# Optimization experiments

Hardware: AMD Instinct MI355X
Metric: run time of the kernel (lower is better)

Reference implementation:

```python
import jax, jax.numpy as jnp
import numpy as np

BETA = 0.25

def setup_inputs() -> dict:
    key = jax.random.key(0)
    k1, k2 = jax.random.split(key)
    x = jax.random.normal(k1, (16, 32, 32, 256), dtype=jnp.float32)
    embed = jax.random.normal(k2, (256, 8192), dtype=jnp.float32)
    return {"x": x, "embed": embed}

def reference(x, embed):
    dim = embed.shape[0]
    flatten = x.reshape(-1, dim)  # [N, dim]
    # squared L2 distance to each code: ||f||^2 - 2 f.e + ||e||^2 -> [N, n_embed]
    dist = (jnp.sum(flatten * flatten, axis=1, keepdims=True)
            - 2.0 * (flatten @ embed)
            + jnp.sum(embed * embed, axis=0, keepdims=True))
    ind = jnp.argmin(dist, axis=1)  # == argmax(-dist)
    embed_ind = ind.reshape(x.shape[:-1])  # [B, H, W]
    codebook = embed.T  # [n_embed, dim]
    quantize = codebook[embed_ind]  # gather -> [B, H, W, dim]
    diff = jnp.mean((jax.lax.stop_gradient(quantize) - x) ** 2)
    commit_loss = jnp.mean((quantize - jax.lax.stop_gradient(x)) ** 2)
    diff = diff + commit_loss * BETA
    quantize = x + jax.lax.stop_gradient(quantize - x)  # straight-through
    return quantize, diff, embed_ind
```

## Files before the change

### kernel.cpp

```cpp
#include <hip/hip_runtime.h>

static constexpr int DIM   = 256;
static constexpr int NCODE = 8192;
static constexpr int NROWS = 16384;

typedef __bf16 bf16x8 __attribute__((ext_vector_type(8)));
typedef float  f32x4  __attribute__((ext_vector_type(4)));

__device__ __forceinline__ void top2_insert(float& v0, int& i0, float& v1, int& i1,
                                            float s, int si) {
    if (s < v0) { v1 = v0; i1 = i0; v0 = s; i0 = si; }
    else if (s < v1) { v1 = s; i1 = si; }
}
__device__ __forceinline__ void top2_merge(float& v0, int& i0, float& v1, int& i1,
                                           float b0, int bi0, float b1, int bi1) {
    if (b0 < v0) {
        if (b1 < v0) { v0 = b0; i0 = bi0; v1 = b1; i1 = bi1; }
        else         { v1 = v0; i1 = i0;  v0 = b0; i0 = bi0; }
    } else if (b0 < v1) { v1 = b0; i1 = bi0; }
}

__global__ __launch_bounds__(256) void prep_kernel(
    const float* __restrict__ x, const float* __restrict__ embed,
    ushort* __restrict__ xb, ushort* __restrict__ eb16,
    float* __restrict__ ebT32, float* __restrict__ e2)
{
    __shared__ float tile[64][65];
    const int b = blockIdx.x;
    const int t = threadIdx.x;

    if (b < 2048) {
        int i = b * 256 + t;
        const float4* xp = (const float4*)x + (size_t)i * 2;
        float4 a = xp[0], v = xp[1];
        bf16x8 o;
        o[0] = (__bf16)a.x; o[1] = (__bf16)a.y; o[2] = (__bf16)a.z; o[3] = (__bf16)a.w;
        o[4] = (__bf16)v.x; o[5] = (__bf16)v.y; o[6] = (__bf16)v.z; o[7] = (__bf16)v.w;
        ((bf16x8*)xb)[i] = o;
    } else if (b < 2560) {
        const int eb = b - 2048;
        const int c00 = (eb & 127) * 64;
        const int k0  = (eb >> 7) * 64;
        const int tc  = t & 63, tr4 = t >> 6;
        #pragma unroll
        for (int i = 0; i < 16; ++i) {
            int r = i * 4 + tr4;
            tile[r][tc] = embed[(size_t)(k0 + r) * NCODE + c00 + tc];
        }
        __syncthreads();
        const int cl = t >> 2;
        const int kq = t & 3;
        float vals[16];
        #pragma unroll
        for (int j = 0; j < 16; ++j) vals[j] = tile[kq * 16 + j][cl];
        float* d32 = ebT32 + (size_t)(c00 + cl) * DIM + k0 + kq * 16;
        #pragma unroll
        for (int j = 0; j < 4; ++j)
            *(float4*)(d32 + j * 4) = make_float4(vals[j*4], vals[j*4+1],
                                                  vals[j*4+2], vals[j*4+3]);
        bf16x8 h0, h1;
        #pragma unroll
        for (int j = 0; j < 8; ++j) { h0[j] = (__bf16)vals[j]; h1[j] = (__bf16)vals[8 + j]; }
        ushort* d16 = eb16 + (size_t)(c00 + cl) * DIM + k0 + kq * 16;
        *(bf16x8*)d16 = h0;
        *(bf16x8*)(d16 + 8) = h1;
    } else {
        int j = (b - 2560) * 256 + t;
        float s = 0.f;
        for (int k = 0; k < DIM; ++k) {
            float v = embed[(size_t)k * NCODE + j];
            s = __fadd_rn(s, __fmul_rn(v, v));
        }
        e2[j] = s;
    }
}

__global__ __launch_bounds__(512, 1) void gemm_top2_kernel(
    const ushort* __restrict__ xb,
    const ushort* __restrict__ eb,
    const float* __restrict__ e2g,
    uint2* __restrict__ scratch)
{
    __shared__ ushort Bs[32768];
    __shared__ ushort As[2][16384];
    __shared__ uint4  ldsM[4][64];

    const int t       = threadIdx.x;
    const int chunk   = blockIdx.x >> 2;
    const int rg      = blockIdx.x & 3;
    const int c0      = chunk * 128;
    const int rowbase = rg * 4096;

    const int wid = t >> 6, lane = t & 63;
    const int wr  = wid >> 2, wc = wid & 3;
    const int lr  = lane & 15, g = lane >> 4;

    {
        const char* bb = (const char*)(eb + (size_t)c0 * DIM);
        uint4 breg[8];
        #pragma unroll
        for (int i = 0; i < 8; ++i)
            breg[i] = *(const uint4*)(bb + i * 8192 + t * 16);
        const char* ab = (const char*)(xb + (size_t)rowbase * DIM);
        uint4 areg[4];
        #pragma unroll
        for (int i = 0; i < 4; ++i)
            areg[i] = *(const uint4*)(ab + i * 8192 + t * 16);
        #pragma unroll
        for (int i = 0; i < 8; ++i) {
            int o = i * 8192 + t * 16;
            int code = o >> 9, kg = (o >> 4) & 31;
            *(uint4*)((char*)Bs + kg * 2048 + (((code ^ kg) & 127) << 4)) = breg[i];
        }
        #pragma unroll
        for (int i = 0; i < 4; ++i) {
            int o = i * 8192 + t * 16;
            int row = o >> 9, kg = (o >> 4) & 31;
            *(uint4*)((char*)As[0] + kg * 1024 + (((row ^ kg) & 63) << 4)) = areg[i];
        }
    }
    __syncthreads();

    bf16x8 bq[2][8];
    #pragma unroll
    for (int cf = 0; cf < 2; ++cf) {
        #pragma unroll
        for (int ks = 0; ks < 8; ++ks) {
            int code = wc * 32 + cf * 16 + lr;
            int kg   = ks * 4 + g;
            bq[cf][ks] = *(const bf16x8*)((char*)Bs + kg * 2048 +
                                          (((code ^ kg) & 127) << 4));
        }
    }

    float e2v[2][4];
    #pragma unroll
    for (int cf = 0; cf < 2; ++cf)
        #pragma unroll
        for (int reg = 0; reg < 4; ++reg)
            e2v[cf][reg] = e2g[c0 + wc * 32 + cf * 16 + g * 4 + reg];

    int cur = 0;
    for (int tt = 0; tt < 64; ++tt) {
        uint4 nreg[4];
        if (tt < 63) {
            const char* an = (const char*)(xb + (size_t)(rowbase + (tt + 1) * 64) * DIM);
            #pragma unroll
            for (int i = 0; i < 4; ++i)
                nreg[i] = *(const uint4*)(an + i * 8192 + t * 16);
        }

        f32x4 acc[2][2];
        #pragma unroll
        for (int cf = 0; cf < 2; ++cf)
            #pragma unroll
            for (int rf = 0; rf < 2; ++rf) acc[cf][rf] = (f32x4){0.f, 0.f, 0.f, 0.f};

        const char* Ab = (const char*)As[cur];
        #pragma unroll
        for (int ks = 0; ks < 8; ++ks) {
            bf16x8 af[2];
            #pragma unroll
            for (int rf = 0; rf < 2; ++rf) {
                int row = wr * 32 + rf * 16 + lr;
                int kg  = ks * 4 + g;
                af[rf] = *(const bf16x8*)(Ab + kg * 1024 + (((row ^ kg) & 63) << 4));
            }
            #pragma unroll
            for (int cf = 0; cf < 2; ++cf)
                #pragma unroll
                for (int rf = 0; rf < 2; ++rf)
                    acc[cf][rf] = __builtin_amdgcn_mfma_f32_16x16x32_bf16(
                        bq[cf][ks], af[rf], acc[cf][rf], 0, 0, 0);
        }

        #pragma unroll
        for (int rf = 0; rf < 2; ++rf) {
            float v0 = __builtin_inff(), v1 = __builtin_inff();
            int   i0 = -1, i1 = -1;
            #pragma unroll
            for (int cf = 0; cf < 2; ++cf) {
                #pragma unroll
                for (int reg = 0; reg < 4; ++reg) {
                    float sv = __builtin_fmaf(-2.f, acc[cf][rf][reg], e2v[cf][reg]);
                    top2_insert(v0, i0, v1, i1, sv,
                                c0 + wc * 32 + cf * 16 + g * 4 + reg);
                }
            }
            #pragma unroll
            for (int m = 16; m <= 32; m <<= 1) {
                float b0 = __shfl_xor(v0, m), b1 = __shfl_xor(v1, m);
                int  bi0 = __shfl_xor(i0, m), bi1 = __shfl_xor(i1, m);
                top2_merge(v0, i0, v1, i1, b0, bi0, b1, bi1);
            }
            if (g == 0)
                ldsM[wc][wr * 32 + rf * 16 + lr] =
                    make_uint4(__float_as_uint(v0), (unsigned)i0,
                               __float_as_uint(v1), (unsigned)i1);
        }
        __syncthreads();

        if (t < 64) {
            uint4 E = ldsM[0][t];
            float v0 = __uint_as_float(E.x), v1 = __uint_as_float(E.z);
            int   i0 = (int)E.y,             i1 = (int)E.w;
            #pragma unroll
            for (int k = 1; k < 4; ++k) {
                uint4 F = ldsM[k][t];
                top2_merge(v0, i0, v1, i1, __uint_as_float(F.x), (int)F.y,
                           __uint_as_float(F.z), (int)F.w);
            }
            float delta = v1 - v0;
            unsigned dq = (unsigned)min(63, (int)(delta * 32.f));
            unsigned w2 = (unsigned)i0 | ((unsigned)i1 << 13) | (dq << 26);
            scratch[(size_t)chunk * NROWS + rowbase + tt * 64 + t] =
                make_uint2(__float_as_uint(v0), w2);
        }

        if (tt < 63) {
            #pragma unroll
            for (int i = 0; i < 4; ++i) {
                int o = i * 8192 + t * 16;
                int row = o >> 9, kg = (o >> 4) & 31;
                *(uint4*)((char*)As[cur ^ 1] + kg * 1024 +
                          (((row ^ kg) & 63) << 4)) = nreg[i];
            }
        }
        __syncthreads();
        cur ^= 1;
    }
}

__global__ __launch_bounds__(256) void finalize_kernel(
    const uint2* __restrict__ scratch, const float* __restrict__ x,
    const float* __restrict__ ebT32, const float* __restrict__ e2g,
    float* __restrict__ quant, float* __restrict__ diff, float* __restrict__ ind)
{
    __shared__ float    wmin[4][64];
    __shared__ float    thr[64];
    __shared__ unsigned cnt[64];
    __shared__ unsigned cand[64][12];
    __shared__ unsigned bestIdx[64];
    __shared__ float    partial[4];

    const int t  = threadIdx.x;
    const int w  = t >> 6, l = t & 63;
    const int R0 = blockIdx.x * 64;

    if (t < 64) cnt[t] = 0;

    float m = __builtin_inff();
    #pragma unroll 4
    for (int i = 0; i < 16; ++i) {
        uint2 e = scratch[(size_t)(w * 16 + i) * NROWS + R0 + l];
        m = fminf(m, __uint_as_float(e.x));
    }
    wmin[w][l] = m;
    __syncthreads();
    if (t < 64)
        thr[t] = fminf(fminf(wmin[0][t], wmin[1][t]),
                       fminf(wmin[2][t], wmin[3][t])) + 1.0f;
    __syncthreads();

    const float th = thr[l];
    for (int i = 0; i < 16; ++i) {
        uint2 e = scratch[(size_t)(w * 16 + i) * NROWS + R0 + l];
        float v0 = __uint_as_float(e.x);
        if (v0 <= th) {
            unsigned s = atomicAdd(&cnt[l], 1u);
            if (s < 12) cand[l][s] = e.y & 8191u;
        }
        float v1lo = v0 + (float)((e.y >> 26) & 63u) * 0.03125f;
        if (v1lo <= th) {
            unsigned s = atomicAdd(&cnt[l], 1u);
            if (s < 12) cand[l][s] = (e.y >> 13) & 8191u;
        }
    }
    __syncthreads();

    const int rl = l >> 2, slot = l & 3;
    const int rrow = R0 + w * 16 + rl;
    const int cn = min((int)cnt[w * 16 + rl], 12);
    float best = __builtin_inff();
    unsigned bidx = 0xFFFFFFFFu;
    for (int s = slot; s < cn; s += 4) {
        unsigned idx = cand[w * 16 + rl][s];
        const float* xr = x + (size_t)rrow * DIM;
        const float* er = ebT32 + (size_t)idx * DIM;
        float f2 = 0.f, dot = 0.f;
        for (int k = 0; k < DIM; ++k) {
            float xv = xr[k];
            f2  = __fadd_rn(f2, __fmul_rn(xv, xv));
            dot = __builtin_fmaf(xv, er[k], dot);
        }
        float d = __fadd_rn(__builtin_fmaf(-2.f, dot, f2), e2g[idx]);
        if (d < best || (d == best && idx < bidx)) { best = d; bidx = idx; }
    }
    #pragma unroll
    for (int mm = 1; mm < 4; mm <<= 1) {
        float    od = __shfl_xor(best, mm);
        unsigned oi = (unsigned)__shfl_xor((int)bidx, mm);
        if (od < best || (od == best && oi < bidx)) { best = od; bidx = oi; }
    }
    if (slot == 0) bestIdx[w * 16 + rl] = bidx;
    __syncthreads();

    float accv = 0.f;
    for (int r = 0; r < 64; ++r) {
        const int row2 = R0 + r;
        const unsigned idx = bestIdx[r];
        float xv = x[(size_t)row2 * DIM + t];
        float q  = ebT32[(size_t)idx * DIM + t];
        float dq = __fsub_rn(q, xv);
        quant[(size_t)row2 * DIM + t] = __fadd_rn(xv, dq);
        accv += __fmul_rn(dq, dq);
    }
    #pragma unroll
    for (int off = 32; off >= 1; off >>= 1) accv += __shfl_down(accv, off);
    if (l == 0) partial[w] = accv;
    __syncthreads();
    if (t == 0) {
        float s = (partial[0] + partial[1]) + (partial[2] + partial[3]);
        atomicAdd(diff, s * (1.25f / 4194304.f));
    }
    if (t < 64) ind[R0 + t] = (float)bestIdx[t];
}

extern "C" void kernel_launch(void* const* d_in, const int* in_sizes, int n_in,
                              void* d_out, int out_size, void* d_ws, size_t ws_size,
                              hipStream_t stream)
{
    const float* x     = (const float*)d_in[0];
    const float* embed = (const float*)d_in[1];

    float* out   = (float*)d_out;
    float* quant = out;
    float* diff  = out + 4194304;
    float* ind   = out + 4194305;

    ushort* xb = (ushort*)quant;

    char* w = (char*)d_ws;
    ushort* eb16    = (ushort*)(w);
    float*  ebT32   = (float*) (w + 4194304);
    float*  e2      = (float*) (w + 12582912);
    uint2*  scratch = (uint2*) (w + 12615680);

    prep_kernel<<<2592, 256, 0, stream>>>(x, embed, xb, eb16, ebT32, e2);
    gemm_top2_kernel<<<256, 512, 0, stream>>>(xb, eb16, e2, scratch);
    hipMemsetAsync(diff, 0, sizeof(float), stream);
    finalize_kernel<<<256, 256, 0, stream>>>(scratch, x, ebT32, e2, quant, diff, ind);
}
```

Before: 706.1 us.

## Restructure GEMM to per-wave top2 with direct global A loads

The GEMM kernel is reorganized into 256-thread blocks, two per CU, each holding a 128-code B tile. Each wave keeps 64 codes in registers and reads A fragments straight from global/L2 instead of double-buffered LDS. Each wave now writes its own top-2 result to scratch, which drops the cross-wave LDS merge and its two barriers per tile but doubles the scratch entries the finalize kernel must scan. The fp32 transposed embedding copy is removed, so finalize reads the original embed with strided column accesses, trading prep write traffic for uncoalesced gathers.

```diff
diff --git a/kernel.cpp b/kernel.cpp
--- a/kernel.cpp
+++ b/kernel.cpp
@@ -22,8 +22,7 @@
 
 __global__ __launch_bounds__(256) void prep_kernel(
     const float* __restrict__ x, const float* __restrict__ embed,
-    ushort* __restrict__ xb, ushort* __restrict__ eb16,
-    float* __restrict__ ebT32, float* __restrict__ e2)
+    ushort* __restrict__ xb, ushort* __restrict__ eb16, float* __restrict__ e2)
 {
     __shared__ float tile[64][65];
     const int b = blockIdx.x;
@@ -53,11 +52,6 @@
         float vals[16];
         #pragma unroll
         for (int j = 0; j < 16; ++j) vals[j] = tile[kq * 16 + j][cl];
-        float* d32 = ebT32 + (size_t)(c00 + cl) * DIM + k0 + kq * 16;
-        #pragma unroll
-        for (int j = 0; j < 4; ++j)
-            *(float4*)(d32 + j * 4) = make_float4(vals[j*4], vals[j*4+1],
-                                                  vals[j*4+2], vals[j*4+3]);
         bf16x8 h0, h1;
         #pragma unroll
         for (int j = 0; j < 8; ++j) { h0[j] = (__bf16)vals[j]; h1[j] = (__bf16)vals[8 + j]; }
@@ -75,103 +69,88 @@
     }
 }
 
-__global__ __launch_bounds__(512, 1) void gemm_top2_kernel(
+__global__ __launch_bounds__(256, 2) void gemm_top2_kernel(
     const ushort* __restrict__ xb,
     const ushort* __restrict__ eb,
     const float* __restrict__ e2g,
     uint2* __restrict__ scratch)
 {
     __shared__ ushort Bs[32768];
-    __shared__ ushort As[2][16384];
-    __shared__ uint4  ldsM[4][64];
 
     const int t       = threadIdx.x;
-    const int chunk   = blockIdx.x >> 2;
-    const int rg      = blockIdx.x & 3;
-    const int c0      = chunk * 128;
-    const int rowbase = rg * 4096;
+    const int cpair   = blockIdx.x >> 3;
+    const int rg      = blockIdx.x & 7;
+    const int c0      = cpair * 128;
+    const int rowbase = rg * 2048;
 
     const int wid = t >> 6, lane = t & 63;
-    const int wr  = wid >> 2, wc = wid & 3;
+    const int wr  = wid >> 1, wc = wid & 1;
     const int lr  = lane & 15, g = lane >> 4;
 
     {
         const char* bb = (const char*)(eb + (size_t)c0 * DIM);
-        uint4 breg[8];
-        #pragma unroll
-        for (int i = 0; i < 8; ++i)
-            breg[i] = *(const uint4*)(bb + i * 8192 + t * 16);
-        const char* ab = (const char*)(xb + (size_t)rowbase * DIM);
-        uint4 areg[4];
-        #pragma unroll
-        for (int i = 0; i < 4; ++i)
-            areg[i] = *(const uint4*)(ab + i * 8192 + t * 16);
-        #pragma unroll
-        for (int i = 0; i < 8; ++i) {
-            int o = i * 8192 + t * 16;
+        uint4 breg[16];
+        #pragma unroll
+        for (int i = 0; i < 16; ++i)
+            breg[i] = *(const uint4*)(bb + i * 4096 + t * 16);
+        #pragma unroll
+        for (int i = 0; i < 16; ++i) {
+            int o = i * 4096 + t * 16;
             int code = o >> 9, kg = (o >> 4) & 31;
-            *(uint4*)((char*)Bs + kg * 2048 + (((code ^ kg) & 127) << 4)) = breg[i];
-        }
-        #pragma unroll
-        for (int i = 0; i < 4; ++i) {
-            int o = i * 8192 + t * 16;
-            int row = o >> 9, kg = (o >> 4) & 31;
-            *(uint4*)((char*)As[0] + kg * 1024 + (((row ^ kg) & 63) << 4)) = areg[i];
-        }
-    }
-    __syncthreads();
-
-    bf16x8 bq[2][8];
+            *(uint4*)((char*)Bs + kg * 2048 + (((code + kg) & 127) << 4)) = breg[i];
+        }
+    }
+    __syncthreads();
+
+    bf16x8 bq[4][8];
     #pragma unroll
-    for (int cf = 0; cf < 2; ++cf) {
+    for (int cf = 0; cf < 4; ++cf) {
         #pragma unroll
         for (int ks = 0; ks < 8; ++ks) {
-            int code = wc * 32 + cf * 16 + lr;
-            int kg   = ks * 4 + g;
+            int codeL = wc * 64 + cf * 16 + lr;
+            int kg    = ks * 4 + g;
             bq[cf][ks] = *(const bf16x8*)((char*)Bs + kg * 2048 +
-                                          (((code ^ kg) & 127) << 4));
-        }
-    }
-
-    float e2v[2][4];
+                                          (((codeL + kg) & 127) << 4));
+        }
+    }
+
+    float e2v[4][4];
     #pragma unroll
-    for (int cf = 0; cf < 2; ++cf)
+    for (int cf = 0; cf < 4; ++cf)
         #pragma unroll
         for (int reg = 0; reg < 4; ++reg)
-            e2v[cf][reg] = e2g[c0 + wc * 32 + cf * 16 + g * 4 + reg];
-
-    int cur = 0;
-    for (int tt = 0; tt < 64; ++tt) {
-        uint4 nreg[4];
-        if (tt < 63) {
-            const char* an = (const char*)(xb + (size_t)(rowbase + (tt + 1) * 64) * DIM);
-            #pragma unroll
-            for (int i = 0; i < 4; ++i)
-                nreg[i] = *(const uint4*)(an + i * 8192 + t * 16);
-        }
-
-        f32x4 acc[2][2];
-        #pragma unroll
-        for (int cf = 0; cf < 2; ++cf)
+            e2v[cf][reg] = e2g[c0 + wc * 64 + cf * 16 + g * 4 + reg];
+
+    const char* ab    = (const char*)xb;
+    const int   ccol  = cpair * 2 + wc;
+
+    for (int tt = 0; tt < 32; ++tt) {
+        const int row0 = rowbase + tt * 64 + wr * 32;
+
+        f32x4 acc[4][2];
+        #pragma unroll
+        for (int cf = 0; cf < 4; ++cf)
             #pragma unroll
             for (int rf = 0; rf < 2; ++rf) acc[cf][rf] = (f32x4){0.f, 0.f, 0.f, 0.f};
 
-        const char* Ab = (const char*)As[cur];
-        #pragma unroll
-        for (int ks = 0; ks < 8; ++ks) {
-            bf16x8 af[2];
-            #pragma unroll
-            for (int rf = 0; rf < 2; ++rf) {
-                int row = wr * 32 + rf * 16 + lr;
-                int kg  = ks * 4 + g;
-                af[rf] = *(const bf16x8*)(Ab + kg * 1024 + (((row ^ kg) & 63) << 4));
-            }
-            #pragma unroll
-            for (int cf = 0; cf < 2; ++cf)
+        #pragma unroll
+        for (int half = 0; half < 2; ++half) {
+            bf16x8 af[4][2];
+            #pragma unroll
+            for (int k4 = 0; k4 < 4; ++k4)
                 #pragma unroll
                 for (int rf = 0; rf < 2; ++rf)
-                    acc[cf][rf] = __builtin_amdgcn_mfma_f32_16x16x32_bf16(
-                        bq[cf][ks], af[rf], acc[cf][rf], 0, 0, 0);
+                    af[k4][rf] = *(const bf16x8*)(ab +
+                        (size_t)(row0 + rf * 16 + lr) * 512 +
+                        (half * 4 + k4) * 64 + g * 16);
+            #pragma unroll
+            for (int k4 = 0; k4 < 4; ++k4)
+                #pragma unroll
+                for (int cf = 0; cf < 4; ++cf)
+                    #pragma unroll
+                    for (int rf = 0; rf < 2; ++rf)
+                        acc[cf][rf] = __builtin_amdgcn_mfma_f32_16x16x32_bf16(
+                            bq[cf][half * 4 + k4], af[k4][rf], acc[cf][rf], 0, 0, 0);
         }
 
         #pragma unroll
@@ -179,12 +158,12 @@
             float v0 = __builtin_inff(), v1 = __builtin_inff();
             int   i0 = -1, i1 = -1;
             #pragma unroll
-            for (int cf = 0; cf < 2; ++cf) {
+            for (int cf = 0; cf < 4; ++cf) {
                 #pragma unroll
                 for (int reg = 0; reg < 4; ++reg) {
                     float sv = __builtin_fmaf(-2.f, acc[cf][rf][reg], e2v[cf][reg]);
                     top2_insert(v0, i0, v1, i1, sv,
-                                c0 + wc * 32 + cf * 16 + g * 4 + reg);
+                                c0 + wc * 64 + cf * 16 + g * 4 + reg);
                 }
             }
             #pragma unroll
@@ -193,47 +172,20 @@
                 int  bi0 = __shfl_xor(i0, m), bi1 = __shfl_xor(i1, m);
                 top2_merge(v0, i0, v1, i1, b0, bi0, b1, bi1);
             }
-            if (g == 0)
-                ldsM[wc][wr * 32 + rf * 16 + lr] =
-                    make_uint4(__float_as_uint(v0), (unsigned)i0,
-                               __float_as_uint(v1), (unsigned)i1);
-        }
-        __syncthreads();
-
-        if (t < 64) {
-            uint4 E = ldsM[0][t];
-            float v0 = __uint_as_float(E.x), v1 = __uint_as_float(E.z);
-            int   i0 = (int)E.y,             i1 = (int)E.w;
-            #pragma unroll
-            for (int k = 1; k < 4; ++k) {
-                uint4 F = ldsM[k][t];
-                top2_merge(v0, i0, v1, i1, __uint_as_float(F.x), (int)F.y,
-                           __uint_as_float(F.z), (int)F.w);
+            if (g == 0) {
+                float delta = v1 - v0;
+                unsigned dq = (unsigned)min(63, (int)(delta * 32.f));
+                unsigned w2 = (unsigned)i0 | ((unsigned)i1 << 13) | (dq << 26);
+                scratch[(size_t)ccol * NROWS + row0 + rf * 16 + lr] =
+                    make_uint2(__float_as_uint(v0), w2);
             }
-            float delta = v1 - v0;
-            unsigned dq = (unsigned)min(63, (int)(delta * 32.f));
-            unsigned w2 = (unsigned)i0 | ((unsigned)i1 << 13) | (dq << 26);
-            scratch[(size_t)chunk * NROWS + rowbase + tt * 64 + t] =
-                make_uint2(__float_as_uint(v0), w2);
-        }
-
-        if (tt < 63) {
-            #pragma unroll
-            for (int i = 0; i < 4; ++i) {
-                int o = i * 8192 + t * 16;
-                int row = o >> 9, kg = (o >> 4) & 31;
-                *(uint4*)((char*)As[cur ^ 1] + kg * 1024 +
-                          (((row ^ kg) & 63) << 4)) = nreg[i];
-            }
-        }
-        __syncthreads();
-        cur ^= 1;
+        }
     }
 }
 
 __global__ __launch_bounds__(256) void finalize_kernel(
     const uint2* __restrict__ scratch, const float* __restrict__ x,
-    const float* __restrict__ ebT32, const float* __restrict__ e2g,
+    const float* __restrict__ embed, const float* __restrict__ e2g,
     float* __restrict__ quant, float* __restrict__ diff, float* __restrict__ ind)
 {
     __shared__ float    wmin[4][64];
@@ -251,8 +203,8 @@
 
     float m = __builtin_inff();
     #pragma unroll 4
-    for (int i = 0; i < 16; ++i) {
-        uint2 e = scratch[(size_t)(w * 16 + i) * NROWS + R0 + l];
+    for (int i = 0; i < 32; ++i) {
+        uint2 e = scratch[(size_t)(w * 32 + i) * NROWS + R0 + l];
         m = fminf(m, __uint_as_float(e.x));
     }
     wmin[w][l] = m;
@@ -263,8 +215,8 @@
     __syncthreads();
 
     const float th = thr[l];
-    for (int i = 0; i < 16; ++i) {
-        uint2 e = scratch[(size_t)(w * 16 + i) * NROWS + R0 + l];
+    for (int i = 0; i < 32; ++i) {
+        uint2 e = scratch[(size_t)(w * 32 + i) * NROWS + R0 + l];
         float v0 = __uint_as_float(e.x);
         if (v0 <= th) {
             unsigned s = atomicAdd(&cnt[l], 1u);
@@ -286,12 +238,11 @@
     for (int s = slot; s < cn; s += 4) {
         unsigned idx = cand[w * 16 + rl][s];
         const float* xr = x + (size_t)rrow * DIM;
-        const float* er = ebT32 + (size_t)idx * DIM;
         float f2 = 0.f, dot = 0.f;
         for (int k = 0; k < DIM; ++k) {
             float xv = xr[k];
             f2  = __fadd_rn(f2, __fmul_rn(xv, xv));
-            dot = __builtin_fmaf(xv, er[k], dot);
+            dot = __builtin_fmaf(xv, embed[(size_t)k * NCODE + idx], dot);
         }
         float d = __fadd_rn(__builtin_fmaf(-2.f, dot, f2), e2g[idx]);
         if (d < best || (d == best && idx < bidx)) { best = d; bidx = idx; }
@@ -310,7 +261,7 @@
         const int row2 = R0 + r;
         const unsigned idx = bestIdx[r];
         float xv = x[(size_t)row2 * DIM + t];
-        float q  = ebT32[(size_t)idx * DIM + t];
+        float q  = embed[(size_t)t * NCODE + idx];
         float dq = __fsub_rn(q, xv);
         quant[(size_t)row2 * DIM + t] = __fadd_rn(xv, dq);
         accv += __fmul_rn(dq, dq);
@@ -342,12 +293,11 @@
 
     char* w = (char*)d_ws;
     ushort* eb16    = (ushort*)(w);
-    float*  ebT32   = (float*) (w + 4194304);
-    float*  e2      = (float*) (w + 12582912);
-    uint2*  scratch = (uint2*) (w + 12615680);
-
-    prep_kernel<<<2592, 256, 0, stream>>>(x, embed, xb, eb16, ebT32, e2);
-    gemm_top2_kernel<<<256, 512, 0, stream>>>(xb, eb16, e2, scratch);
+    uint2*  scratch = (uint2*) (w + 4194304);
+    float*  e2      = (float*) (w + 20971520);
+
+    prep_kernel<<<2592, 256, 0, stream>>>(x, embed, xb, eb16, e2);
+    gemm_top2_kernel<<<512, 256, 0, stream>>>(xb, eb16, e2, scratch);
     hipMemsetAsync(diff, 0, sizeof(float), stream);
-    finalize_kernel<<<256, 256, 0, stream>>>(scratch, x, ebT32, e2, quant, diff, ind);
-}
+    finalize_kernel<<<256, 256, 0, stream>>>(scratch, x, embed, e2, quant, diff, ind);
+}
```

After: 669.1 us. 1.06x faster.
